# Kernel tuning notes

Measured on AMD Instinct MI355X. Metric: run time of the kernel, lower is better.

## Reference

```python
import jax, jax.numpy as jnp
import numpy as np
import math

N = 50000
E = 1_600_000
F_IN = 512
F_OUT = 256
TAO = 3.0


def setup_inputs() -> dict:
    key = jax.random.key(0)
    ks = jax.random.split(key, 12)
    stdv = 1.0 / math.sqrt(F_OUT)
    std_att = 1.0 / math.sqrt(F_OUT)
    std_att_vec = 1.0 / math.sqrt(3)
    inp = {
        "inputx": jax.random.normal(ks[0], (N, F_IN), dtype=jnp.float32),
        "adj_row": jax.random.randint(ks[1], (E,), 0, N, dtype=jnp.int32),
        "adj_col": jax.random.randint(ks[2], (E,), 0, N, dtype=jnp.int32),
        "adj_val": jax.random.uniform(ks[3], (E,), dtype=jnp.float32),
        "sadj_row": jax.random.randint(ks[4], (E,), 0, N, dtype=jnp.int32),
        "sadj_col": jax.random.randint(ks[5], (E,), 0, N, dtype=jnp.int32),
        "sadj_val": jax.random.uniform(ks[6], (E,), dtype=jnp.float32),
        "weight_mlp": jax.random.uniform(ks[7], (F_IN, F_OUT), minval=-stdv, maxval=stdv, dtype=jnp.float32),
        "weight_A": jax.random.uniform(ks[8], (F_IN, F_OUT), minval=-stdv, maxval=stdv, dtype=jnp.float32),
        "weight_As": jax.random.uniform(ks[9], (F_IN, F_OUT), minval=-stdv, maxval=stdv, dtype=jnp.float32),
        "att_vec_k": jax.random.uniform(ks[10], (F_OUT, F_OUT), minval=-std_att, maxval=std_att, dtype=jnp.float32),
        "att_vec_v": jax.random.uniform(ks[11], (3, 3), minval=-std_att_vec, maxval=std_att_vec, dtype=jnp.float32),
    }
    return inp


def _spmm(row, col, val, h):
    # sparse [N,N] @ dense [N,F]: gather source rows, scale, scatter-add to dest
    msgs = val[:, None] * h[col]  # [E, F]
    return jax.ops.segment_sum(msgs, row, num_segments=N)


def reference(inputx, adj_row, adj_col, adj_val, sadj_row, sadj_col, sadj_val,
              weight_mlp, weight_A, weight_As, att_vec_k, att_vec_v):
    output_mlp = jax.nn.relu(inputx @ weight_mlp)                     # [N, F]
    output_A = jax.nn.relu(_spmm(adj_row, adj_col, adj_val, inputx @ weight_A))
    output_As = jax.nn.relu(_spmm(sadj_row, sadj_col, sadj_val, inputx @ weight_As))

    output_stru = output_mlp + output_As + output_A
    K = jnp.mean(output_stru @ att_vec_k, axis=0, keepdims=True)      # [1, F]
    logits = jnp.concatenate([output_mlp @ K.T, output_A @ K.T, output_As @ K.T], axis=1)  # [N, 3]
    att = jax.nn.softmax((jax.nn.sigmoid(logits) @ att_vec_v) / TAO, axis=1)
    alpha_mlp, alpha_A, alpha_As = att[:, 0:1], att[:, 1:2], att[:, 2:3]
    emb = alpha_mlp * output_mlp + alpha_A * output_A + alpha_As * output_As
    return emb
```

## Files before the change

kernel.cpp:

```cpp
#include <hip/hip_runtime.h>
#include <hip/hip_bf16.h>

#define N_NODES 50000
#define E_EDGES 1600000
#define FIN 512
#define FOUT 256
#define NCOMB 768
#define TAO_F 3.0f
#define M_PAD 50048
#define NB 196
#define CSTRIDE 16
#define CH 4096

typedef __bf16 bf16x8 __attribute__((ext_vector_type(8)));
typedef float  f32x4  __attribute__((ext_vector_type(4)));

static __device__ __forceinline__ unsigned short f2bf(float f) {
    unsigned int u = __float_as_uint(f);
    u += 0x7FFFu + ((u >> 16) & 1u);
    return (unsigned short)(u >> 16);
}
static __device__ __forceinline__ float bf2f(unsigned short h) {
    return __uint_as_float(((unsigned int)h) << 16);
}

__global__ void convert_x_kernel(const float* __restrict__ X, unsigned short* __restrict__ Xb) {
    long long i = ((long long)blockIdx.x * blockDim.x + threadIdx.x) * 4;
    const long long total = (long long)M_PAD * FIN;
    if (i >= total) return;
    const long long valid = (long long)N_NODES * FIN;
    ushort4 o;
    if (i < valid) {
        const float4 v = *reinterpret_cast<const float4*>(X + i);
        o.x = f2bf(v.x); o.y = f2bf(v.y); o.z = f2bf(v.z); o.w = f2bf(v.w);
    } else {
        o.x = o.y = o.z = o.w = 0;
    }
    *reinterpret_cast<ushort4*>(Xb + i) = o;
}

__global__ void convert_w_kernel(const float* __restrict__ Wm, const float* __restrict__ Wa,
                                 const float* __restrict__ Was, unsigned short* __restrict__ Wt) {
    int i = blockIdx.x * blockDim.x + threadIdx.x;
    if (i >= NCOMB * FIN) return;
    int row = i / FIN, k = i % FIN;
    int w = row >> 8, n = row & 255;
    const float* W = (w == 0) ? Wm : (w == 1) ? Wa : Was;
    Wt[i] = f2bf(W[(size_t)k * FOUT + n]);
}

#define BM 128
#define BN 128
#define BK 64
#define LDSTR 72

__global__ __launch_bounds__(256) void gemm_kernel(const unsigned short* __restrict__ A,
                                                   const unsigned short* __restrict__ Bt,
                                                   float* __restrict__ Omlp,
                                                   unsigned short* __restrict__ HA,
                                                   unsigned short* __restrict__ HAs) {
    __shared__ unsigned short As[BM * LDSTR];
    __shared__ unsigned short Bs[BN * LDSTR];
    const int tid = threadIdx.x;
    const int lane = tid & 63, wave = tid >> 6;
    const int wr = wave >> 1, wc = wave & 1;
    const int row0 = blockIdx.y * BM, col0 = blockIdx.x * BN;
    f32x4 acc[4][4] = {};

    for (int k0 = 0; k0 < FIN; k0 += BK) {
#pragma unroll
        for (int i = 0; i < 4; i++) {
            int chunk = tid + i * 256;
            int r = chunk >> 3, kc = chunk & 7;
            *reinterpret_cast<bf16x8*>(&As[r * LDSTR + kc * 8]) =
                *reinterpret_cast<const bf16x8*>(A + (size_t)(row0 + r) * FIN + k0 + kc * 8);
            *reinterpret_cast<bf16x8*>(&Bs[r * LDSTR + kc * 8]) =
                *reinterpret_cast<const bf16x8*>(Bt + (size_t)(col0 + r) * FIN + k0 + kc * 8);
        }
        __syncthreads();
#pragma unroll
        for (int kk = 0; kk < 2; kk++) {
            bf16x8 af[4], bfr[4];
            const int ko = kk * 32 + (lane >> 4) * 8;
#pragma unroll
            for (int m = 0; m < 4; m++)
                af[m] = *reinterpret_cast<const bf16x8*>(&As[(wr * 64 + m * 16 + (lane & 15)) * LDSTR + ko]);
#pragma unroll
            for (int n = 0; n < 4; n++)
                bfr[n] = *reinterpret_cast<const bf16x8*>(&Bs[(wc * 64 + n * 16 + (lane & 15)) * LDSTR + ko]);
#pragma unroll
            for (int m = 0; m < 4; m++)
#pragma unroll
                for (int n = 0; n < 4; n++)
                    acc[m][n] = __builtin_amdgcn_mfma_f32_16x16x32_bf16(af[m], bfr[n], acc[m][n], 0, 0, 0);
        }
        __syncthreads();
    }

    const int seg = col0 >> 8;
    unsigned short* hp = (seg == 1) ? HA : HAs;
    const int rb = row0 + wr * 64 + ((lane >> 4) << 2);
    const int cb = col0 + wc * 64 + (lane & 15) - seg * 256;
#pragma unroll
    for (int m = 0; m < 4; m++)
#pragma unroll
        for (int n = 0; n < 4; n++)
#pragma unroll
            for (int j = 0; j < 4; j++) {
                int r = rb + m * 16 + j;
                if (r < N_NODES) {
                    float v = acc[m][n][j];
                    int c = cb + n * 16;
                    if (seg == 0) Omlp[(size_t)r * FOUT + c] = fmaxf(v, 0.f);
                    else          hp[(size_t)r * FOUT + c] = f2bf(v);
                }
            }
}

__global__ __launch_bounds__(256) void hist_kernel(const int* __restrict__ rowA, int* __restrict__ bcntA,
                                                   const int* __restrict__ rowS, int* __restrict__ bcntS) {
    __shared__ int h[2 * NB];
    const int t = threadIdx.x;
    for (int j = t; j < 2 * NB; j += 256) h[j] = 0;
    __syncthreads();
    int i = blockIdx.x * blockDim.x + t;
    const int stride = gridDim.x * blockDim.x;
    for (; i < E_EDGES; i += stride) {
        atomicAdd(&h[rowA[i] >> 8], 1);
        atomicAdd(&h[NB + (rowS[i] >> 8)], 1);
    }
    __syncthreads();
    for (int j = t; j < 2 * NB; j += 256) {
        int v = h[j];
        if (v) {
            if (j < NB) atomicAdd(&bcntA[j * CSTRIDE], v);
            else        atomicAdd(&bcntS[(j - NB) * CSTRIDE], v);
        }
    }
}

__global__ __launch_bounds__(256) void scan196_kernel(const int* __restrict__ bcntA, int* __restrict__ bstartA,
                                                      int* __restrict__ bcurA,
                                                      const int* __restrict__ bcntS, int* __restrict__ bstartS,
                                                      int* __restrict__ bcurS) {
    __shared__ int wsum[4];
    const int t = threadIdx.x, lane = t & 63, w = t >> 6;
    for (int g = 0; g < 2; g++) {
        const int* bcnt = g ? bcntS : bcntA;
        int* bstart = g ? bstartS : bstartA;
        int* bcur = g ? bcurS : bcurA;
        int v = (t < NB) ? bcnt[t * CSTRIDE] : 0;
        int x = v;
#pragma unroll
        for (int off = 1; off < 64; off <<= 1) { int y = __shfl_up(x, off); if (lane >= off) x += y; }
        if (lane == 63) wsum[w] = x;
        __syncthreads();
        int woff = 0;
        for (int i = 0; i < w; i++) woff += wsum[i];
        int ex = woff + x - v;
        if (t < NB) { bstart[t] = ex; bcur[t * CSTRIDE] = ex; }
        if (t == 0) bstart[NB] = E_EDGES;
        __syncthreads();
    }
}

__global__ __launch_bounds__(256) void pass1_kernel(
    const int* __restrict__ rowA, const int* __restrict__ colA, const float* __restrict__ valA,
    int* __restrict__ bcurA, int2* __restrict__ ed1A,
    const int* __restrict__ rowS, const int* __restrict__ colS, const float* __restrict__ valS,
    int* __restrict__ bcurS, int2* __restrict__ ed1S) {
    __shared__ int lcnt[NB];
    __shared__ int gcur[NB];
    const int t = threadIdx.x;
    const int base = blockIdx.x * CH;
    const int n = min(CH, E_EDGES - base);
    for (int g = 0; g < 2; g++) {
        const int* row = g ? rowS : rowA;
        const int* col = g ? colS : colA;
        const float* val = g ? valS : valA;
        int* bcur = g ? bcurS : bcurA;
        int2* ed1 = g ? ed1S : ed1A;
        for (int j = t; j < NB; j += 256) lcnt[j] = 0;
        __syncthreads();
        for (int j = t; j < n; j += 256) atomicAdd(&lcnt[row[base + j] >> 8], 1);
        __syncthreads();
        for (int j = t; j < NB; j += 256) {
            int c = lcnt[j];
            gcur[j] = c ? atomicAdd(&bcur[j * CSTRIDE], c) : 0;
        }
        __syncthreads();
        for (int j = t; j < n; j += 256) {
            int r = row[base + j];
            int b = r >> 8;
            int pos = atomicAdd(&gcur[b], 1);
            ed1[pos] = make_int2(((r & 255) << 16) | col[base + j], __float_as_int(val[base + j]));
        }
        __syncthreads();
    }
}

__global__ __launch_bounds__(256) void pass2_kernel(
    const int* __restrict__ bstartA, const int2* __restrict__ ed1A, int2* __restrict__ ed2A, int* __restrict__ rpA,
    const int* __restrict__ bstartS, const int2* __restrict__ ed1S, int2* __restrict__ ed2S, int* __restrict__ rpS) {
    const int g = (blockIdx.x >= NB) ? 1 : 0;
    const int b = blockIdx.x - g * NB;
    const int* bstart = g ? bstartS : bstartA;
    const int2* ed1 = g ? ed1S : ed1A;
    int2* ed2 = g ? ed2S : ed2A;
    int* rp = g ? rpS : rpA;
    const int s = bstart[b], e = bstart[b + 1];
    const int t = threadIdx.x, lane = t & 63, w = t >> 6;
    __shared__ int rcnt[256];
    __shared__ int lcur[256];
    __shared__ int wsum[4];
    rcnt[t] = 0;
    __syncthreads();
    for (int j = s + t; j < e; j += 256) atomicAdd(&rcnt[ed1[j].x >> 16], 1);
    __syncthreads();
    const int v = rcnt[t];
    int x = v;
#pragma unroll
    for (int off = 1; off < 64; off <<= 1) { int y = __shfl_up(x, off); if (lane >= off) x += y; }
    if (lane == 63) wsum[w] = x;
    __syncthreads();
    int woff = 0;
    for (int i = 0; i < w; i++) woff += wsum[i];
    const int ex = woff + x - v;
    const int row = b * 256 + t;
    if (row < N_NODES) rp[row] = s + ex;
    if (b == NB - 1 && t == 0) rp[N_NODES] = E_EDGES;
    lcur[t] = ex;
    __syncthreads();
    for (int j = s + t; j < e; j += 256) {
        int2 v2 = ed1[j];
        int rl = v2.x >> 16;
        int k = atomicAdd(&lcur[rl], 1);
        ed2[s + k] = make_int2(v2.x & 0xFFFF, v2.y);
    }
}

__global__ __launch_bounds__(256) void spmm_kernel(
    const int* __restrict__ rpA, const int2* __restrict__ edA,
    const unsigned short* __restrict__ HA, float* __restrict__ OA,
    const int* __restrict__ rpS, const int2* __restrict__ edS,
    const unsigned short* __restrict__ HS, float* __restrict__ OS) {
    const int gw = blockIdx.x * 4 + (threadIdx.x >> 6);
    const int lane = threadIdx.x & 63;
    const int* rp; const int2* ed; const unsigned short* H; float* O; int r;
    if (gw < N_NODES) { rp = rpA; ed = edA; H = HA; O = OA; r = gw; }
    else              { rp = rpS; ed = edS; H = HS; O = OS; r = gw - N_NODES; }
    const int s = rp[r], e = rp[r + 1];
    float a0 = 0.f, a1 = 0.f, a2 = 0.f, a3 = 0.f;
#pragma unroll 4
    for (int i = s; i < e; ++i) {
        const int2 ev = ed[i];
        const float v = __int_as_float(ev.y);
        const uint2 hv = *reinterpret_cast<const uint2*>(H + (((size_t)ev.x) << 8) + lane * 4);
        a0 += v * bf2f((unsigned short)(hv.x & 0xFFFFu));
        a1 += v * bf2f((unsigned short)(hv.x >> 16));
        a2 += v * bf2f((unsigned short)(hv.y & 0xFFFFu));
        a3 += v * bf2f((unsigned short)(hv.y >> 16));
    }
    float4 o = make_float4(fmaxf(a0, 0.f), fmaxf(a1, 0.f), fmaxf(a2, 0.f), fmaxf(a3, 0.f));
    *reinterpret_cast<float4*>(O + (((size_t)r) << 8) + lane * 4) = o;
}

__global__ void colsum_kernel(const float* __restrict__ Om, const float* __restrict__ Oa,
                              const float* __restrict__ Oas, float* __restrict__ colsum) {
    const int t = threadIdx.x;
    float acc = 0.f;
    for (int r = blockIdx.x; r < N_NODES; r += gridDim.x) {
        size_t o = (size_t)r * FOUT + t;
        acc += Om[o] + Oa[o] + Oas[o];
    }
    atomicAdd(&colsum[t], acc);
}

__global__ void kvec_kernel(const float* __restrict__ colsum, const float* __restrict__ attk,
                            float* __restrict__ Kv) {
    __shared__ float mean_s[FOUT];
    const int t = threadIdx.x;
    mean_s[t] = colsum[t] * (1.0f / (float)N_NODES);
    __syncthreads();
    float acc = 0.f;
    for (int i = 0; i < FOUT; i++) acc += mean_s[i] * attk[(size_t)i * FOUT + t];
    Kv[t] = acc;
}

__global__ __launch_bounds__(256) void final_kernel(float* __restrict__ OmOut, const float* __restrict__ Oa,
                                                    const float* __restrict__ Oas, const float* __restrict__ Kv,
                                                    const float* __restrict__ attv) {
    const int r = blockIdx.x, t = threadIdx.x, lane = t & 63, w = t >> 6;
    __shared__ float red[4][3];
    __shared__ float alpha[3];
    const size_t o = (size_t)r * FOUT + t;
    const float om = OmOut[o], oa = Oa[o], oas = Oas[o];
    const float kv = Kv[t];
    float p0 = om * kv, p1 = oa * kv, p2 = oas * kv;
#pragma unroll
    for (int off = 32; off; off >>= 1) {
        p0 += __shfl_down(p0, off);
        p1 += __shfl_down(p1, off);
        p2 += __shfl_down(p2, off);
    }
    if (lane == 0) { red[w][0] = p0; red[w][1] = p1; red[w][2] = p2; }
    __syncthreads();
    if (t == 0) {
        float l0 = red[0][0] + red[1][0] + red[2][0] + red[3][0];
        float l1 = red[0][1] + red[1][1] + red[2][1] + red[3][1];
        float l2 = red[0][2] + red[1][2] + red[2][2] + red[3][2];
        float s0 = 1.f / (1.f + __expf(-l0));
        float s1 = 1.f / (1.f + __expf(-l1));
        float s2 = 1.f / (1.f + __expf(-l2));
        float q0 = (s0 * attv[0] + s1 * attv[3] + s2 * attv[6]) * (1.f / TAO_F);
        float q1 = (s0 * attv[1] + s1 * attv[4] + s2 * attv[7]) * (1.f / TAO_F);
        float q2 = (s0 * attv[2] + s1 * attv[5] + s2 * attv[8]) * (1.f / TAO_F);
        float mx = fmaxf(q0, fmaxf(q1, q2));
        float e0 = __expf(q0 - mx), e1 = __expf(q1 - mx), e2 = __expf(q2 - mx);
        float inv = 1.f / (e0 + e1 + e2);
        alpha[0] = e0 * inv; alpha[1] = e1 * inv; alpha[2] = e2 * inv;
    }
    __syncthreads();
    OmOut[o] = alpha[0] * om + alpha[1] * oa + alpha[2] * oas;
}

extern "C" void kernel_launch(void* const* d_in, const int* in_sizes, int n_in,
                              void* d_out, int out_size, void* d_ws, size_t ws_size,
                              hipStream_t stream) {
    (void)in_sizes; (void)n_in; (void)out_size; (void)ws_size;
    const float* X        = (const float*)d_in[0];
    const int*   adj_row  = (const int*)d_in[1];
    const int*   adj_col  = (const int*)d_in[2];
    const float* adj_val  = (const float*)d_in[3];
    const int*   sadj_row = (const int*)d_in[4];
    const int*   sadj_col = (const int*)d_in[5];
    const float* sadj_val = (const float*)d_in[6];
    const float* W_mlp    = (const float*)d_in[7];
    const float* W_A      = (const float*)d_in[8];
    const float* W_As     = (const float*)d_in[9];
    const float* attk     = (const float*)d_in[10];
    const float* attv     = (const float*)d_in[11];
    float* out = (float*)d_out;

    char* p = (char*)d_ws;
    auto alloc = [&](size_t bytes) -> char* {
        char* q = p; p += (bytes + 255) & ~(size_t)255; return q;
    };
    unsigned short* Xb   = (unsigned short*)alloc((size_t)M_PAD * FIN * 2);
    unsigned short* Wt   = (unsigned short*)alloc((size_t)NCOMB * FIN * 2);
    unsigned short* H_A  = (unsigned short*)alloc((size_t)N_NODES * FOUT * 2);
    unsigned short* H_As = (unsigned short*)alloc((size_t)N_NODES * FOUT * 2);
    float* O_A   = (float*)alloc((size_t)N_NODES * FOUT * 4);
    float* O_As  = (float*)alloc((size_t)N_NODES * FOUT * 4);
    int2*  ed1A  = (int2*)alloc((size_t)E_EDGES * 8);
    int2*  ed1S  = (int2*)alloc((size_t)E_EDGES * 8);
    int2*  ed2A  = (int2*)alloc((size_t)E_EDGES * 8);
    int2*  ed2S  = (int2*)alloc((size_t)E_EDGES * 8);
    int*   bcntA = (int*)alloc((size_t)NB * CSTRIDE * 4);
    int*   bcntS = (int*)alloc((size_t)NB * CSTRIDE * 4);
    int*   bcurA = (int*)alloc((size_t)NB * CSTRIDE * 4);
    int*   bcurS = (int*)alloc((size_t)NB * CSTRIDE * 4);
    int*   bstartA = (int*)alloc((size_t)(NB + 1) * 4);
    int*   bstartS = (int*)alloc((size_t)(NB + 1) * 4);
    int*   rpA   = (int*)alloc((size_t)(N_NODES + 1) * 4);
    int*   rpS   = (int*)alloc((size_t)(N_NODES + 1) * 4);
    float* colsum = (float*)alloc(FOUT * 4);
    float* Kv     = (float*)alloc(FOUT * 4);

    hipMemsetAsync(bcntA, 0, (size_t)NB * CSTRIDE * 4, stream);
    hipMemsetAsync(bcntS, 0, (size_t)NB * CSTRIDE * 4, stream);
    hipMemsetAsync(colsum, 0, FOUT * 4, stream);

    {
        long long total = (long long)M_PAD * FIN / 4;
        int blocks = (int)((total + 255) / 256);
        convert_x_kernel<<<blocks, 256, 0, stream>>>(X, Xb);
    }
    convert_w_kernel<<<(NCOMB * FIN + 255) / 256, 256, 0, stream>>>(W_mlp, W_A, W_As, Wt);

    hist_kernel<<<512, 256, 0, stream>>>(adj_row, bcntA, sadj_row, bcntS);
    scan196_kernel<<<1, 256, 0, stream>>>(bcntA, bstartA, bcurA, bcntS, bstartS, bcurS);
    pass1_kernel<<<(E_EDGES + CH - 1) / CH, 256, 0, stream>>>(
        adj_row, adj_col, adj_val, bcurA, ed1A,
        sadj_row, sadj_col, sadj_val, bcurS, ed1S);
    pass2_kernel<<<2 * NB, 256, 0, stream>>>(bstartA, ed1A, ed2A, rpA,
                                             bstartS, ed1S, ed2S, rpS);

    dim3 ggrid(NCOMB / BN, M_PAD / BM);
    gemm_kernel<<<ggrid, 256, 0, stream>>>(Xb, Wt, out, H_A, H_As);

    spmm_kernel<<<(2 * N_NODES) / 4, 256, 0, stream>>>(rpA, ed2A, H_A, O_A, rpS, ed2S, H_As, O_As);

    colsum_kernel<<<512, 256, 0, stream>>>(out, O_A, O_As, colsum);
    kvec_kernel<<<1, 256, 0, stream>>>(colsum, attk, Kv);
    final_kernel<<<N_NODES, 256, 0, stream>>>(out, O_A, O_As, Kv, attv);
}
```

Measured before the change: 561.2 us.

## Use direct global-to-LDS loads in GEMM, sort edges by column chunk, store SpMM outputs as bf16

The GEMM tile staging now uses global_load_lds to write global data straight into unpadded LDS, so the data no longer passes through registers. The second CSR build pass sorts each row's edges by column chunk so the SpMM gathers touch H with better locality. The SpMM outputs O_A and O_As are stored in bf16 instead of fp32, which halves their write and later read traffic in colsum and the final kernel. The unpadded LDS layout can cause bank conflicts on fragment reads, the larger LDS histograms in pass2 lower occupancy, and the bf16 outputs lose precision.

Result: no change. 560.0 us (-0.2%).

```diff
diff --git a/kernel.cpp b/kernel.cpp
--- a/kernel.cpp
+++ b/kernel.cpp
@@ -11,6 +11,7 @@
 #define NB 196
 #define CSTRIDE 16
 #define CH 4096
+#define NCH 13
 
 typedef __bf16 bf16x8 __attribute__((ext_vector_type(8)));
 typedef float  f32x4  __attribute__((ext_vector_type(4)));
@@ -52,30 +53,34 @@
 #define BM 128
 #define BN 128
 #define BK 64
-#define LDSTR 72
 
 __global__ __launch_bounds__(256) void gemm_kernel(const unsigned short* __restrict__ A,
                                                    const unsigned short* __restrict__ Bt,
                                                    float* __restrict__ Omlp,
                                                    unsigned short* __restrict__ HA,
                                                    unsigned short* __restrict__ HAs) {
-    __shared__ unsigned short As[BM * LDSTR];
-    __shared__ unsigned short Bs[BN * LDSTR];
+    __shared__ unsigned short As[BM * BK];
+    __shared__ unsigned short Bs[BN * BK];
     const int tid = threadIdx.x;
     const int lane = tid & 63, wave = tid >> 6;
     const int wr = wave >> 1, wc = wave & 1;
     const int row0 = blockIdx.y * BM, col0 = blockIdx.x * BN;
+    const int st_row = tid >> 3;
+    const int st_col = (tid & 7) * 8;
+    const int lds_off = wave * 512;
+    const unsigned short* Ag = A + (size_t)(row0 + st_row) * FIN + st_col;
+    const unsigned short* Bg = Bt + (size_t)(col0 + st_row) * FIN + st_col;
     f32x4 acc[4][4] = {};
 
     for (int k0 = 0; k0 < FIN; k0 += BK) {
 #pragma unroll
         for (int i = 0; i < 4; i++) {
-            int chunk = tid + i * 256;
-            int r = chunk >> 3, kc = chunk & 7;
-            *reinterpret_cast<bf16x8*>(&As[r * LDSTR + kc * 8]) =
-                *reinterpret_cast<const bf16x8*>(A + (size_t)(row0 + r) * FIN + k0 + kc * 8);
-            *reinterpret_cast<bf16x8*>(&Bs[r * LDSTR + kc * 8]) =
-                *reinterpret_cast<const bf16x8*>(Bt + (size_t)(col0 + r) * FIN + k0 + kc * 8);
+            __builtin_amdgcn_global_load_lds(
+                (const __attribute__((address_space(1))) unsigned int*)(Ag + (size_t)i * 32 * FIN + k0),
+                (__attribute__((address_space(3))) unsigned int*)&As[i * 2048 + lds_off], 16, 0, 0);
+            __builtin_amdgcn_global_load_lds(
+                (const __attribute__((address_space(1))) unsigned int*)(Bg + (size_t)i * 32 * FIN + k0),
+                (__attribute__((address_space(3))) unsigned int*)&Bs[i * 2048 + lds_off], 16, 0, 0);
         }
         __syncthreads();
 #pragma unroll
@@ -84,10 +89,10 @@
             const int ko = kk * 32 + (lane >> 4) * 8;
 #pragma unroll
             for (int m = 0; m < 4; m++)
-                af[m] = *reinterpret_cast<const bf16x8*>(&As[(wr * 64 + m * 16 + (lane & 15)) * LDSTR + ko]);
+                af[m] = *reinterpret_cast<const bf16x8*>(&As[(wr * 64 + m * 16 + (lane & 15)) * BK + ko]);
 #pragma unroll
             for (int n = 0; n < 4; n++)
-                bfr[n] = *reinterpret_cast<const bf16x8*>(&Bs[(wc * 64 + n * 16 + (lane & 15)) * LDSTR + ko]);
+                bfr[n] = *reinterpret_cast<const bf16x8*>(&Bs[(wc * 64 + n * 16 + (lane & 15)) * BK + ko]);
 #pragma unroll
             for (int m = 0; m < 4; m++)
 #pragma unroll
@@ -210,43 +215,50 @@
     int* rp = g ? rpS : rpA;
     const int s = bstart[b], e = bstart[b + 1];
     const int t = threadIdx.x, lane = t & 63, w = t >> 6;
-    __shared__ int rcnt[256];
-    __shared__ int lcur[256];
+    __shared__ int rcnt[256 * NCH];
+    __shared__ int lcur[256 * NCH];
     __shared__ int wsum[4];
-    rcnt[t] = 0;
-    __syncthreads();
-    for (int j = s + t; j < e; j += 256) atomicAdd(&rcnt[ed1[j].x >> 16], 1);
-    __syncthreads();
-    const int v = rcnt[t];
-    int x = v;
+    for (int j = t; j < 256 * NCH; j += 256) rcnt[j] = 0;
+    __syncthreads();
+    for (int j = s + t; j < e; j += 256) {
+        int2 v2 = ed1[j];
+        atomicAdd(&rcnt[(v2.x >> 16) * NCH + ((v2.x & 0xFFFF) >> 12)], 1);
+    }
+    __syncthreads();
+    int rsum = 0;
+#pragma unroll
+    for (int c = 0; c < NCH; c++) rsum += rcnt[t * NCH + c];
+    int x = rsum;
 #pragma unroll
     for (int off = 1; off < 64; off <<= 1) { int y = __shfl_up(x, off); if (lane >= off) x += y; }
     if (lane == 63) wsum[w] = x;
     __syncthreads();
     int woff = 0;
     for (int i = 0; i < w; i++) woff += wsum[i];
-    const int ex = woff + x - v;
+    const int ex = woff + x - rsum;
     const int row = b * 256 + t;
     if (row < N_NODES) rp[row] = s + ex;
     if (b == NB - 1 && t == 0) rp[N_NODES] = E_EDGES;
-    lcur[t] = ex;
+    int off2 = ex;
+#pragma unroll
+    for (int c = 0; c < NCH; c++) { lcur[t * NCH + c] = off2; off2 += rcnt[t * NCH + c]; }
     __syncthreads();
     for (int j = s + t; j < e; j += 256) {
         int2 v2 = ed1[j];
-        int rl = v2.x >> 16;
-        int k = atomicAdd(&lcur[rl], 1);
+        int rl = v2.x >> 16, cc = (v2.x & 0xFFFF) >> 12;
+        int k = atomicAdd(&lcur[rl * NCH + cc], 1);
         ed2[s + k] = make_int2(v2.x & 0xFFFF, v2.y);
     }
 }
 
 __global__ __launch_bounds__(256) void spmm_kernel(
     const int* __restrict__ rpA, const int2* __restrict__ edA,
-    const unsigned short* __restrict__ HA, float* __restrict__ OA,
+    const unsigned short* __restrict__ HA, unsigned short* __restrict__ OA,
     const int* __restrict__ rpS, const int2* __restrict__ edS,
-    const unsigned short* __restrict__ HS, float* __restrict__ OS) {
+    const unsigned short* __restrict__ HS, unsigned short* __restrict__ OS) {
     const int gw = blockIdx.x * 4 + (threadIdx.x >> 6);
     const int lane = threadIdx.x & 63;
-    const int* rp; const int2* ed; const unsigned short* H; float* O; int r;
+    const int* rp; const int2* ed; const unsigned short* H; unsigned short* O; int r;
     if (gw < N_NODES) { rp = rpA; ed = edA; H = HA; O = OA; r = gw; }
     else              { rp = rpS; ed = edS; H = HS; O = OS; r = gw - N_NODES; }
     const int s = rp[r], e = rp[r + 1];
@@ -261,17 +273,21 @@
         a2 += v * bf2f((unsigned short)(hv.y & 0xFFFFu));
         a3 += v * bf2f((unsigned short)(hv.y >> 16));
     }
-    float4 o = make_float4(fmaxf(a0, 0.f), fmaxf(a1, 0.f), fmaxf(a2, 0.f), fmaxf(a3, 0.f));
-    *reinterpret_cast<float4*>(O + (((size_t)r) << 8) + lane * 4) = o;
-}
-
-__global__ void colsum_kernel(const float* __restrict__ Om, const float* __restrict__ Oa,
-                              const float* __restrict__ Oas, float* __restrict__ colsum) {
+    ushort4 o;
+    o.x = f2bf(fmaxf(a0, 0.f));
+    o.y = f2bf(fmaxf(a1, 0.f));
+    o.z = f2bf(fmaxf(a2, 0.f));
+    o.w = f2bf(fmaxf(a3, 0.f));
+    *reinterpret_cast<ushort4*>(O + (((size_t)r) << 8) + lane * 4) = o;
+}
+
+__global__ void colsum_kernel(const float* __restrict__ Om, const unsigned short* __restrict__ Oa,
+                              const unsigned short* __restrict__ Oas, float* __restrict__ colsum) {
     const int t = threadIdx.x;
     float acc = 0.f;
     for (int r = blockIdx.x; r < N_NODES; r += gridDim.x) {
         size_t o = (size_t)r * FOUT + t;
-        acc += Om[o] + Oa[o] + Oas[o];
+        acc += Om[o] + bf2f(Oa[o]) + bf2f(Oas[o]);
     }
     atomicAdd(&colsum[t], acc);
 }
@@ -287,14 +303,14 @@
     Kv[t] = acc;
 }
 
-__global__ __launch_bounds__(256) void final_kernel(float* __restrict__ OmOut, const float* __restrict__ Oa,
-                                                    const float* __restrict__ Oas, const float* __restrict__ Kv,
+__global__ __launch_bounds__(256) void final_kernel(float* __restrict__ OmOut, const unsigned short* __restrict__ Oa,
+                                                    const unsigned short* __restrict__ Oas, const float* __restrict__ Kv,
                                                     const float* __restrict__ attv) {
     const int r = blockIdx.x, t = threadIdx.x, lane = t & 63, w = t >> 6;
     __shared__ float red[4][3];
     __shared__ float alpha[3];
     const size_t o = (size_t)r * FOUT + t;
-    const float om = OmOut[o], oa = Oa[o], oas = Oas[o];
+    const float om = OmOut[o], oa = bf2f(Oa[o]), oas = bf2f(Oas[o]);
     const float kv = Kv[t];
     float p0 = om * kv, p1 = oa * kv, p2 = oas * kv;
 #pragma unroll
@@ -350,8 +366,8 @@
     unsigned short* Wt   = (unsigned short*)alloc((size_t)NCOMB * FIN * 2);
     unsigned short* H_A  = (unsigned short*)alloc((size_t)N_NODES * FOUT * 2);
     unsigned short* H_As = (unsigned short*)alloc((size_t)N_NODES * FOUT * 2);
-    float* O_A   = (float*)alloc((size_t)N_NODES * FOUT * 4);
-    float* O_As  = (float*)alloc((size_t)N_NODES * FOUT * 4);
+    unsigned short* O_A  = (unsigned short*)alloc((size_t)N_NODES * FOUT * 2);
+    unsigned short* O_As = (unsigned short*)alloc((size_t)N_NODES * FOUT * 2);
     int2*  ed1A  = (int2*)alloc((size_t)E_EDGES * 8);
     int2*  ed1S  = (int2*)alloc((size_t)E_EDGES * 8);
     int2*  ed2A  = (int2*)alloc((size_t)E_EDGES * 8);
```
